# Kernel tuning notes

Measured on AMD Instinct MI355X. Metric: run time of the kernel, lower is better.

The kernel has to match this reference:

```python
import jax, jax.numpy as jnp
import numpy as np

B, T_PREFIX, C_IN = 8, 6144, 8
OUT_LEN, OUT_C = 2048, 8
AUX_DIM = 16
D_MODEL, D_STATE, HEADDIM, EXPAND = 256, 32, 64, 2
D_INNER = EXPAND * D_MODEL            # 512
NHEADS = D_INNER // HEADDIM           # 8
CONV_DIM = D_INNER + 2 * D_STATE      # 576
D_PROJ = 2 * D_INNER + 2 * D_STATE + NHEADS  # 1096
N_LAYERS = 2
CHUNK = 64
PATCH = 16
PRECONV_K = 5
DCONV_K = 4


def setup_inputs() -> dict:
    key = jax.random.key(0)
    ks = iter(jax.random.split(key, 64))
    def rn(shape, s=0.02):
        return s * jax.random.normal(next(ks), shape, jnp.float32)
    inp = dict(
        x_prefix=jax.random.normal(next(ks), (B, T_PREFIX, C_IN), jnp.float32),
        y_aux=jax.random.normal(next(ks), (B, AUX_DIM), jnp.float32),
        pre_conv_w=rn((D_MODEL, C_IN, PRECONV_K), 0.1),
        pre_conv_b=rn((D_MODEL,)),
        patch_w=rn((D_MODEL, D_MODEL, PATCH), 0.05),
        patch_b=rn((D_MODEL,)),
        mask_token=rn((D_MODEL,)),
        aux_w=rn((AUX_DIM, D_MODEL), 0.1),
        aux_b=rn((D_MODEL,)),
        patch_out_w=rn((2 * D_MODEL, OUT_C * PATCH), 0.05),
        patch_out_b=rn((OUT_C * PATCH,)),
    )
    for d in ('fwd', 'bwd'):
        inp[f'{d}_norm_w'] = jnp.ones((N_LAYERS, D_MODEL), jnp.float32)
        inp[f'{d}_inproj'] = rn((N_LAYERS, D_MODEL, D_PROJ), 0.05)
        inp[f'{d}_conv_w'] = rn((N_LAYERS, CONV_DIM, DCONV_K), 0.2)
        inp[f'{d}_conv_b'] = rn((N_LAYERS, CONV_DIM))
        inp[f'{d}_dtbias'] = rn((N_LAYERS, NHEADS), 0.5)
        inp[f'{d}_Alog'] = jnp.tile(jnp.log(jnp.arange(1, NHEADS + 1, dtype=jnp.float32)), (N_LAYERS, 1))
        inp[f'{d}_D'] = jnp.ones((N_LAYERS, NHEADS), jnp.float32)
        inp[f'{d}_gnorm'] = jnp.ones((N_LAYERS, D_INNER), jnp.float32)
        inp[f'{d}_outproj'] = rn((N_LAYERS, D_INNER, D_MODEL), 0.05)
    return inp


def rmsnorm(x, w, eps=1e-5):
    return x * jax.lax.rsqrt(jnp.mean(x * x, axis=-1, keepdims=True) + eps) * w


def conv1d(x, w, b, stride, pad):  # x: [B,C,T], w: [O,I,K]
    y = jax.lax.conv_general_dilated(x, w, (stride,), [(pad, pad)],
                                     dimension_numbers=('NCH', 'OIH', 'NCH'))
    return y + b[None, :, None]


def mamba_block(u, inproj, conv_w, conv_b, dtbias, Alog, Dp, gnorm_w, outproj):
    # Mamba-2/SSD style block: in_proj -> z | xBC | dt, causal depthwise conv,
    # selective scan with per-head scalar decay A, +D skip, gated RMSNorm, out_proj.
    b, T, _ = u.shape
    zxbcdt = u @ inproj                                   # [b,T,D_PROJ]
    z = zxbcdt[..., :D_INNER]
    xBC = zxbcdt[..., D_INNER:D_INNER + CONV_DIM]
    dt = jax.nn.softplus(zxbcdt[..., -NHEADS:] + dtbias)  # [b,T,H]
    # causal depthwise conv over time
    xc = jax.lax.conv_general_dilated(xBC.transpose(0, 2, 1), conv_w[:, None, :], (1,),
                                      [(DCONV_K - 1, 0)],
                                      dimension_numbers=('NCH', 'OIH', 'NCH'),
                                      feature_group_count=CONV_DIM)
    xBC = jax.nn.silu((xc + conv_b[None, :, None]).transpose(0, 2, 1))
    xs = xBC[..., :D_INNER].reshape(b, T, NHEADS, HEADDIM)  # [b,T,H,P]
    Bm = xBC[..., D_INNER:D_INNER + D_STATE]                # [b,T,N]
    Cm = xBC[..., D_INNER + D_STATE:]                       # [b,T,N]
    A = -jnp.exp(Alog)                                      # [H]

    def step(h, inps):  # h: [b,H,P,N]
        dt_t, x_t, B_t, C_t = inps
        dA = jnp.exp(dt_t * A)[:, :, None, None]
        h = h * dA + (dt_t[:, :, None] * x_t)[..., None] * B_t[:, None, None, :]
        y = jnp.einsum('bhpn,bn->bhp', h, C_t)
        return h, y

    h0 = jnp.zeros((b, NHEADS, HEADDIM, D_STATE), u.dtype)
    _, ys = jax.lax.scan(step, h0, (dt.transpose(1, 0, 2), xs.transpose(1, 0, 2, 3),
                                    Bm.transpose(1, 0, 2), Cm.transpose(1, 0, 2)))
    y = ys.transpose(1, 0, 2, 3) + Dp[None, None, :, None] * xs
    y = y.reshape(b, T, D_INNER)
    y = rmsnorm(y * jax.nn.silu(z), gnorm_w)
    return y @ outproj


def reference(x_prefix, y_aux, pre_conv_w, pre_conv_b, patch_w, patch_b, mask_token,
              aux_w, aux_b, fwd_norm_w, fwd_inproj, fwd_conv_w, fwd_conv_b, fwd_dtbias,
              fwd_Alog, fwd_D, fwd_gnorm, fwd_outproj, bwd_norm_w, bwd_inproj,
              bwd_conv_w, bwd_conv_b, bwd_dtbias, bwd_Alog, bwd_D, bwd_gnorm,
              bwd_outproj, patch_out_w, patch_out_b):
    b = x_prefix.shape[0]
    t_total = T_PREFIX + OUT_LEN
    x_full = jnp.pad(x_prefix, ((0, 0), (0, OUT_LEN), (0, 0)))        # zeros for future
    x = jax.nn.silu(conv1d(x_full.transpose(0, 2, 1), pre_conv_w, pre_conv_b, 1, PRECONV_K // 2))
    x = conv1d(x, patch_w, patch_b, PATCH, 0).transpose(0, 2, 1)      # [b, n_tokens, d_model]
    n_tokens = x.shape[1]
    # eval mode: deterministic future-patch mask, dropout is identity
    starts = jnp.arange(n_tokens) * PATCH
    mask = (starts >= T_PREFIX)[None, :, None]
    x = jnp.where(mask, mask_token[None, None, :], x)
    aux_bias = jax.nn.silu(y_aux @ aux_w + aux_b)[:, None, :]
    x = x + aux_bias
    pad_t = (-n_tokens) % CHUNK
    if pad_t:
        x = jnp.pad(x, ((0, 0), (0, pad_t), (0, 0)))
    h_f = x
    h_b = x[:, ::-1]
    for i in range(N_LAYERS):
        h_f = h_f + mamba_block(rmsnorm(h_f, fwd_norm_w[i]), fwd_inproj[i], fwd_conv_w[i],
                                fwd_conv_b[i], fwd_dtbias[i], fwd_Alog[i], fwd_D[i],
                                fwd_gnorm[i], fwd_outproj[i])
        h_b = h_b + mamba_block(rmsnorm(h_b, bwd_norm_w[i]), bwd_inproj[i], bwd_conv_w[i],
                                bwd_conv_b[i], bwd_dtbias[i], bwd_Alog[i], bwd_D[i],
                                bwd_gnorm[i], bwd_outproj[i])
    h = jnp.concatenate([h_f, h_b[:, ::-1]], axis=-1)[:, :n_tokens]   # [b,n,2*d_model]
    patch_pred = h @ patch_out_w + patch_out_b                        # [b,n,out_c*patch]
    y = patch_pred.reshape(b, n_tokens, OUT_C, PATCH).reshape(b, n_tokens * PATCH, OUT_C)
    y = y[:, :t_total, :]
    return y[:, T_PREFIX:, :]
```

## Files before the change

### kernel.cpp

```cpp
#include <hip/hip_runtime.h>
#include <hip/hip_bf16.h>
#include <math.h>

#define BSZ      8
#define TPREF    6144
#define CIN      8
#define DMODEL   256
#define DINNER   512
#define DSTATE   32
#define NHEADS   8
#define HEADDIM  64
#define CONVDIM  576
#define DPROJ    1096
#define ZXW      1088
#define NTOK     512
#define NVIS     384
#define TBWD     128
#define MFWD     (BSZ * NTOK)
#define MBWD     (BSZ * TBWD)
#define MALL     (MFWD + MBWD)

typedef float f32x4 __attribute__((ext_vector_type(4)));
typedef __bf16 bf16x8 __attribute__((ext_vector_type(8)));

__device__ __forceinline__ float silu_f(float x) { return x / (1.f + expf(-x)); }

#define ASYNC16(gp, lp) \
    __builtin_amdgcn_global_load_lds((const __attribute__((address_space(1))) void*)(gp), \
                                     (__attribute__((address_space(3))) void*)(lp), 16, 0, 0)

__global__ __launch_bounds__(256) void gemm_mfma(
    const __bf16* __restrict__ A, const __bf16* __restrict__ Bt,
    float* __restrict__ C, const float* __restrict__ bias,
    int N, int K, int ldc, int flags) {
    __shared__ char sm[16384];
    int tid = threadIdx.x;
    int m0 = blockIdx.y * 128, n0 = blockIdx.x * 128;
    int klen = K / gridDim.z;
    int kbeg = blockIdx.z * klen;
    int w = tid >> 6, l = tid & 63;
    int wm = w >> 1, wn = w & 1;
    int lm = l & 15, q = l >> 4;

    f32x4 acc[4][4];
    #pragma unroll
    for (int i = 0; i < 4; i++)
        #pragma unroll
        for (int j = 0; j < 4; j++) acc[i][j] = (f32x4)0.f;

    for (int k0 = 0; k0 < klen; k0 += 32) {
        int kb = kbeg + k0;
        #pragma unroll
        for (int i = 0; i < 2; i++) {
            int s = i * 256 + tid;
            ASYNC16(A + (size_t)(m0 + (s >> 2)) * K + kb + (s & 3) * 8, sm + s * 16);
        }
        #pragma unroll
        for (int i = 0; i < 2; i++) {
            int s = i * 256 + tid;
            ASYNC16(Bt + (size_t)(n0 + (s >> 2)) * K + kb + (s & 3) * 8, sm + 8192 + s * 16);
        }
        __syncthreads();
        bf16x8 af[4], bfr[4];
        #pragma unroll
        for (int mf = 0; mf < 4; mf++)
            af[mf] = *(const bf16x8*)(sm + (wm * 64 + mf * 16 + lm) * 64 + q * 16);
        #pragma unroll
        for (int nf = 0; nf < 4; nf++)
            bfr[nf] = *(const bf16x8*)(sm + 8192 + (wn * 64 + nf * 16 + lm) * 64 + q * 16);
        #pragma unroll
        for (int mf = 0; mf < 4; mf++)
            #pragma unroll
            for (int nf = 0; nf < 4; nf++)
                acc[mf][nf] = __builtin_amdgcn_mfma_f32_16x16x32_bf16(af[mf], bfr[nf], acc[mf][nf], 0, 0, 0);
        __syncthreads();
    }

    #pragma unroll
    for (int mf = 0; mf < 4; mf++) {
        int mbase = m0 + wm * 64 + mf * 16 + q * 4;
        #pragma unroll
        for (int nf = 0; nf < 4; nf++) {
            int n = n0 + wn * 64 + nf * 16 + lm;
            if (n < N) {
                #pragma unroll
                for (int r = 0; r < 4; r++) {
                    float v = acc[mf][nf][r];
                    if (flags & 4) {
                        v = silu_f(v + bias[n]);
                        ((__bf16*)C)[(size_t)(mbase + r) * ldc + n] = (__bf16)v;
                    } else if (flags & 16) {
                        int mm = mbase + r;
                        int bb = mm / NVIS, tk = mm - bb * NVIS;
                        atomicAdd(C + ((size_t)(bb * NTOK + tk)) * 256 + n, v);
                    } else if (flags & 2) {
                        atomicAdd(C + (size_t)(mbase + r) * ldc + n, v);
                    } else {
                        C[(size_t)(mbase + r) * ldc + n] = v;
                    }
                }
            }
        }
    }
}

__global__ __launch_bounds__(256) void preconv_gemm(
    const float* __restrict__ xp, const __bf16* __restrict__ WpreT,
    const float* __restrict__ bias, __bf16* __restrict__ Apatch) {
    __shared__ char sm[32768];
    int tid = threadIdx.x;
    int m0 = blockIdx.y * 128, n0 = blockIdx.x * 128;
    int w = tid >> 6, l = tid & 63;
    int wm = w >> 1, wn = w & 1, lm = l & 15, q = l >> 4;

    #pragma unroll
    for (int i = 0; i < 4; i++) {
        int s = i * 256 + tid;
        int kh = s >> 9, row = (s & 511) >> 2, within = s & 3;
        ASYNC16(WpreT + (size_t)(n0 + row) * 64 + kh * 32 + within * 8, sm + 16384 + s * 16);
    }
    if (tid < 128) {
        int m = m0 + tid;
        int b = m / TPREF, t = m - b * TPREF;
        __bf16 d[64];
        #pragma unroll
        for (int j = 40; j < 64; j++) d[j] = (__bf16)0.f;
        #pragma unroll
        for (int k = 0; k < 5; k++) {
            int tt = t - 2 + k;
            bool ok = (tt >= 0) && (tt < TPREF);
            const float* s = xp + ((size_t)b * TPREF + tt) * 8;
            #pragma unroll
            for (int i = 0; i < 8; i++)
                d[i * 5 + k] = ok ? (__bf16)s[i] : (__bf16)0.f;
        }
        uint4* o0 = (uint4*)(sm + tid * 64);
        uint4* o1 = (uint4*)(sm + 8192 + tid * 64);
        #pragma unroll
        for (int k = 0; k < 4; k++) { o0[k] = ((const uint4*)d)[k]; o1[k] = ((const uint4*)d)[4 + k]; }
    }
    __syncthreads();

    f32x4 acc[4][4];
    #pragma unroll
    for (int i = 0; i < 4; i++)
        #pragma unroll
        for (int j = 0; j < 4; j++) acc[i][j] = (f32x4)0.f;
    #pragma unroll
    for (int kh = 0; kh < 2; kh++) {
        bf16x8 af[4], bfr[4];
        #pragma unroll
        for (int mf = 0; mf < 4; mf++)
            af[mf] = *(const bf16x8*)(sm + kh * 8192 + (wm * 64 + mf * 16 + lm) * 64 + q * 16);
        #pragma unroll
        for (int nf = 0; nf < 4; nf++)
            bfr[nf] = *(const bf16x8*)(sm + 16384 + kh * 8192 + (wn * 64 + nf * 16 + lm) * 64 + q * 16);
        #pragma unroll
        for (int mf = 0; mf < 4; mf++)
            #pragma unroll
            for (int nf = 0; nf < 4; nf++)
                acc[mf][nf] = __builtin_amdgcn_mfma_f32_16x16x32_bf16(af[mf], bfr[nf], acc[mf][nf], 0, 0, 0);
    }
    #pragma unroll
    for (int mf = 0; mf < 4; mf++) {
        int mbase = m0 + wm * 64 + mf * 16 + q * 4;
        #pragma unroll
        for (int nf = 0; nf < 4; nf++) {
            int n = n0 + wn * 64 + nf * 16 + lm;
            #pragma unroll
            for (int r = 0; r < 4; r++) {
                float v = silu_f(acc[mf][nf][r] + bias[n]);
                Apatch[(size_t)(mbase + r) * 256 + n] = (__bf16)v;
            }
        }
    }
}

__global__ __launch_bounds__(256) void final_gemm(
    const float* __restrict__ h_all, const __bf16* __restrict__ poT,
    float* __restrict__ out) {
    __shared__ __bf16 Asm_[128][40];
    __shared__ char Bsm[8192];
    int tid = threadIdx.x;
    int m0 = blockIdx.y * 128;
    int z = blockIdx.z;
    int dir = z >> 1, kh = z & 1;
    int koff = kh * 128;
    int w = tid >> 6, l = tid & 63;
    int wm = w >> 1, wn_ = w & 1, lm = l & 15, q = l >> 4;
    f32x4 acc[4][4];
    #pragma unroll
    for (int i = 0; i < 4; i++)
        #pragma unroll
        for (int j = 0; j < 4; j++) acc[i][j] = (f32x4)0.f;

    int r = tid >> 1, half = tid & 1;
    int m = m0 + r;
    int b = m >> 7, jj = m & 127;
    size_t arow = (dir == 0) ? ((size_t)(b * NTOK + NVIS + jj) * 256)
                             : ((size_t)MFWD * 256 + (size_t)(b * TBWD + (TBWD - 1 - jj)) * 256);
    for (int k0 = 0; k0 < 128; k0 += 32) {
        {
            const float4* sp = (const float4*)(h_all + arow + koff + k0 + half * 16);
            float4 v0 = sp[0], v1 = sp[1], v2 = sp[2], v3 = sp[3];
            union { uint4 u; __bf16 hh[8]; } d0, d1;
            d0.hh[0] = (__bf16)v0.x; d0.hh[1] = (__bf16)v0.y; d0.hh[2] = (__bf16)v0.z; d0.hh[3] = (__bf16)v0.w;
            d0.hh[4] = (__bf16)v1.x; d0.hh[5] = (__bf16)v1.y; d0.hh[6] = (__bf16)v1.z; d0.hh[7] = (__bf16)v1.w;
            d1.hh[0] = (__bf16)v2.x; d1.hh[1] = (__bf16)v2.y; d1.hh[2] = (__bf16)v2.z; d1.hh[3] = (__bf16)v2.w;
            d1.hh[4] = (__bf16)v3.x; d1.hh[5] = (__bf16)v3.y; d1.hh[6] = (__bf16)v3.z; d1.hh[7] = (__bf16)v3.w;
            *(uint4*)&Asm_[r][half * 16] = d0.u;
            *(uint4*)&Asm_[r][half * 16 + 8] = d1.u;
        }
        #pragma unroll
        for (int i = 0; i < 2; i++) {
            int s = i * 256 + tid;
            ASYNC16(poT + (size_t)(s >> 2) * 512 + dir * 256 + koff + k0 + (s & 3) * 8, Bsm + s * 16);
        }
        __syncthreads();
        bf16x8 af[4], bfr[4];
        #pragma unroll
        for (int mf = 0; mf < 4; mf++)
            af[mf] = *(const bf16x8*)&Asm_[wm * 64 + mf * 16 + lm][q * 8];
        #pragma unroll
        for (int nf = 0; nf < 4; nf++)
            bfr[nf] = *(const bf16x8*)(Bsm + (wn_ * 64 + nf * 16 + lm) * 64 + q * 16);
        #pragma unroll
        for (int mf = 0; mf < 4; mf++)
            #pragma unroll
            for (int nf = 0; nf < 4; nf++)
                acc[mf][nf] = __builtin_amdgcn_mfma_f32_16x16x32_bf16(af[mf], bfr[nf], acc[mf][nf], 0, 0, 0);
        __syncthreads();
    }
    #pragma unroll
    for (int mf = 0; mf < 4; mf++) {
        int mbase = m0 + wm * 64 + mf * 16 + q * 4;
        #pragma unroll
        for (int nf = 0; nf < 4; nf++) {
            int n = wn_ * 64 + nf * 16 + lm;
            #pragma unroll
            for (int rr = 0; rr < 4; rr++)
                atomicAdd(out + (size_t)(mbase + rr) * 128 + n, acc[mf][nf][rr]);
        }
    }
}

__global__ __launch_bounds__(256) void gemm_inproj(
    const __bf16* __restrict__ u, const __bf16* __restrict__ ipTf,
    const __bf16* __restrict__ ipTb, __bf16* __restrict__ zxb, float* __restrict__ dtc) {
    __shared__ char sm[16384];
    int tid = threadIdx.x;
    int m0 = blockIdx.y * 128, n0 = blockIdx.x * 128;
    const __bf16* Bt = (m0 >= MFWD) ? ipTb : ipTf;
    int w = tid >> 6, l = tid & 63;
    int wm = w >> 1, wn = w & 1, lm = l & 15, q = l >> 4;
    f32x4 acc[4][4];
    #pragma unroll
    for (int i = 0; i < 4; i++)
        #pragma unroll
        for (int j = 0; j < 4; j++) acc[i][j] = (f32x4)0.f;
    for (int k0 = 0; k0 < 256; k0 += 32) {
        #pragma unroll
        for (int i = 0; i < 2; i++) {
            int s = i * 256 + tid;
            ASYNC16(u + (size_t)(m0 + (s >> 2)) * 256 + k0 + (s & 3) * 8, sm + s * 16);
        }
        #pragma unroll
        for (int i = 0; i < 2; i++) {
            int s = i * 256 + tid;
            ASYNC16(Bt + (size_t)(n0 + (s >> 2)) * 256 + k0 + (s & 3) * 8, sm + 8192 + s * 16);
        }
        __syncthreads();
        bf16x8 af[4], bfr[4];
        #pragma unroll
        for (int mf = 0; mf < 4; mf++)
            af[mf] = *(const bf16x8*)(sm + (wm * 64 + mf * 16 + lm) * 64 + q * 16);
        #pragma unroll
        for (int nf = 0; nf < 4; nf++)
            bfr[nf] = *(const bf16x8*)(sm + 8192 + (wn * 64 + nf * 16 + lm) * 64 + q * 16);
        #pragma unroll
        for (int mf = 0; mf < 4; mf++)
            #pragma unroll
            for (int nf = 0; nf < 4; nf++)
                acc[mf][nf] = __builtin_amdgcn_mfma_f32_16x16x32_bf16(af[mf], bfr[nf], acc[mf][nf], 0, 0, 0);
        __syncthreads();
    }
    #pragma unroll
    for (int mf = 0; mf < 4; mf++) {
        int mbase = m0 + wm * 64 + mf * 16 + q * 4;
        #pragma unroll
        for (int nf = 0; nf < 4; nf++) {
            int n = n0 + wn * 64 + nf * 16 + lm;
            #pragma unroll
            for (int r = 0; r < 4; r++) {
                float v = acc[mf][nf][r];
                if (n < ZXW) zxb[(size_t)(mbase + r) * ZXW + n] = (__bf16)v;
                else if (n < DPROJ) dtc[(size_t)(mbase + r) * 8 + (n - ZXW)] = v;
            }
        }
    }
}

__global__ __launch_bounds__(256) void gemm_outproj(
    const __bf16* __restrict__ y2, const __bf16* __restrict__ opTf,
    const __bf16* __restrict__ opTb, float* __restrict__ C, int layer) {
    __shared__ char sm[16384];
    int tid = threadIdx.x;
    int yb = blockIdx.y;
    int m0 = (layer == 0) ? yb * 128
                          : ((yb < 8) ? (yb * 512 + 384) : (MFWD + (yb - 8) * 128));
    int n0 = blockIdx.x * 128;
    const __bf16* Bt = (m0 >= MFWD) ? opTb : opTf;
    int w = tid >> 6, l = tid & 63;
    int wm = w >> 1, wn = w & 1, lm = l & 15, q = l >> 4;
    f32x4 acc[4][4];
    #pragma unroll
    for (int i = 0; i < 4; i++)
        #pragma unroll
        for (int j = 0; j < 4; j++) acc[i][j] = (f32x4)0.f;
    for (int k0 = 0; k0 < 512; k0 += 32) {
        #pragma unroll
        for (int i = 0; i < 2; i++) {
            int s = i * 256 + tid;
            ASYNC16(y2 + (size_t)(m0 + (s >> 2)) * 512 + k0 + (s & 3) * 8, sm + s * 16);
        }
        #pragma unroll
        for (int i = 0; i < 2; i++) {
            int s = i * 256 + tid;
            ASYNC16(Bt + (size_t)(n0 + (s >> 2)) * 512 + k0 + (s & 3) * 8, sm + 8192 + s * 16);
        }
        __syncthreads();
        bf16x8 af[4], bfr[4];
        #pragma unroll
        for (int mf = 0; mf < 4; mf++)
            af[mf] = *(const bf16x8*)(sm + (wm * 64 + mf * 16 + lm) * 64 + q * 16);
        #pragma unroll
        for (int nf = 0; nf < 4; nf++)
            bfr[nf] = *(const bf16x8*)(sm + 8192 + (wn * 64 + nf * 16 + lm) * 64 + q * 16);
        #pragma unroll
        for (int mf = 0; mf < 4; mf++)
            #pragma unroll
            for (int nf = 0; nf < 4; nf++)
                acc[mf][nf] = __builtin_amdgcn_mfma_f32_16x16x32_bf16(af[mf], bfr[nf], acc[mf][nf], 0, 0, 0);
        __syncthreads();
    }
    #pragma unroll
    for (int mf = 0; mf < 4; mf++) {
        int mbase = m0 + wm * 64 + mf * 16 + q * 4;
        #pragma unroll
        for (int nf = 0; nf < 4; nf++) {
            int n = n0 + wn * 64 + nf * 16 + lm;
            #pragma unroll
            for (int r = 0; r < 4; r++) {
                size_t ci = (size_t)(mbase + r) * DMODEL + n;
                C[ci] += acc[mf][nf][r];
            }
        }
    }
}

__global__ __launch_bounds__(256) void rmsnorm_all(
    const float* __restrict__ h, const float* __restrict__ wf,
    const float* __restrict__ wb, __bf16* __restrict__ u) {
    int row = blockIdx.x * 4 + (threadIdx.x >> 6);
    int lane = threadIdx.x & 63;
    const float* w = (row >= MFWD) ? wb : wf;
    float4 v = ((const float4*)(h + (size_t)row * 256))[lane];
    float ss = v.x * v.x + v.y * v.y + v.z * v.z + v.w * v.w;
    #pragma unroll
    for (int off = 32; off >= 1; off >>= 1) ss += __shfl_xor(ss, off);
    float rs = rsqrtf(ss * (1.f / 256.f) + 1e-5f);
    float4 wv = ((const float4*)w)[lane];
    __bf16 o4[4] = {(__bf16)(v.x * rs * wv.x), (__bf16)(v.y * rs * wv.y),
                    (__bf16)(v.z * rs * wv.z), (__bf16)(v.w * rs * wv.w)};
    *(uint2*)(u + (size_t)row * 256 + lane * 4) = *(uint2*)o4;
}

__global__ __launch_bounds__(256) void gatednorm_all(
    const __bf16* __restrict__ ysD, const __bf16* __restrict__ zxb,
    const float* __restrict__ gwf, const float* __restrict__ gwb,
    __bf16* __restrict__ y2) {
    int row = blockIdx.x * 4 + (threadIdx.x >> 6);
    int lane = threadIdx.x & 63;
    const float* gw = (row >= MFWD) ? gwb : gwf;
    union { uint4 u; __bf16 hh[8]; } yv, zv;
    yv.u = *(const uint4*)(ysD + (size_t)row * 512 + lane * 8);
    zv.u = *(const uint4*)(zxb + (size_t)row * ZXW + lane * 8);
    float g[8];
    #pragma unroll
    for (int j = 0; j < 8; j++) g[j] = (float)yv.hh[j] * silu_f((float)zv.hh[j]);
    float ss = 0.f;
    #pragma unroll
    for (int j = 0; j < 8; j++) ss += g[j] * g[j];
    #pragma unroll
    for (int off = 32; off >= 1; off >>= 1) ss += __shfl_xor(ss, off);
    float rs = rsqrtf(ss * (1.f / 512.f) + 1e-5f);
    const float4* gr = (const float4*)(gw + lane * 8);
    float4 g0 = gr[0], g1 = gr[1];
    union { uint4 u; __bf16 hh[8]; } d;
    d.hh[0] = (__bf16)(g[0] * rs * g0.x); d.hh[1] = (__bf16)(g[1] * rs * g0.y);
    d.hh[2] = (__bf16)(g[2] * rs * g0.z); d.hh[3] = (__bf16)(g[3] * rs * g0.w);
    d.hh[4] = (__bf16)(g[4] * rs * g1.x); d.hh[5] = (__bf16)(g[5] * rs * g1.y);
    d.hh[6] = (__bf16)(g[6] * rs * g1.z); d.hh[7] = (__bf16)(g[7] * rs * g1.w);
    *(uint4*)(y2 + (size_t)row * 512 + lane * 8) = d.u;
}

__global__ void prep_all(const float* __restrict__ pre_conv_w, const float* __restrict__ patch_w,
                         const float* __restrict__ ip0, const float* __restrict__ ip1,
                         const float* __restrict__ op0, const float* __restrict__ op1,
                         const float* __restrict__ pow_, const float* __restrict__ pob,
                         const float* __restrict__ y_aux, const float* __restrict__ aux_w,
                         const float* __restrict__ aux_b,
                         const float* __restrict__ patch_b, const float* __restrict__ mtok,
                         __bf16* __restrict__ WpreT, __bf16* __restrict__ WtT,
                         __bf16* __restrict__ inprojT, __bf16* __restrict__ outprojT,
                         __bf16* __restrict__ poT, float* __restrict__ dout,
                         float* __restrict__ h_all) {
    __shared__ float tile[32][33];
    int bx = blockIdx.x, tid = threadIdx.x;
    int tx = tid & 31, ty = tid >> 5;
    if (bx < 256) {
        int o = bx, c = tid;
        float f[16];
        const float4* s = (const float4*)(patch_w + (size_t)o * 4096 + c * 16);
        #pragma unroll
        for (int j = 0; j < 4; j++) *(float4*)&f[j * 4] = s[j];
        #pragma unroll
        for (int k = 0; k < 16; k++)
            WtT[(size_t)o * 4096 + k * 256 + c] = (__bf16)f[k];
        return;
    }
    bx -= 256;
    if (bx < 1152) {
        int seg = bx / 288, rem = bx % 288;
        int n0 = (rem / 8) * 32, k0 = (rem % 8) * 32;
        const float* src = (seg < 2 ? ip0 : ip1) + (size_t)(seg & 1) * 256 * DPROJ;
        #pragma unroll
        for (int j = 0; j < 4; j++) {
            int r = ty + j * 8;
            int n = n0 + tx;
            tile[r][tx] = (n < DPROJ) ? src[(size_t)(k0 + r) * DPROJ + n] : 0.f;
        }
        __syncthreads();
        __bf16* dst = inprojT + (size_t)seg * 1152 * 256;
        #pragma unroll
        for (int j = 0; j < 4; j++) {
            int r = ty + j * 8;
            dst[(size_t)(n0 + r) * 256 + k0 + tx] = (__bf16)tile[tx][r];
        }
        return;
    }
    bx -= 1152;
    if (bx < 512) {
        int s = bx / 128, rem = bx % 128;
        int n0 = (rem / 16) * 32, k0 = (rem % 16) * 32;
        const float* src = (s < 2 ? op0 : op1) + (size_t)(s & 1) * DINNER * DMODEL;
        #pragma unroll
        for (int j = 0; j < 4; j++) {
            int r = ty + j * 8;
            tile[r][tx] = src[(size_t)(k0 + r) * 256 + n0 + tx];
        }
        __syncthreads();
        __bf16* dst = outprojT + (size_t)s * 256 * 512;
        #pragma unroll
        for (int j = 0; j < 4; j++) {
            int r = ty + j * 8;
            dst[(size_t)(n0 + r) * 512 + k0 + tx] = (__bf16)tile[tx][r];
        }
        return;
    }
    bx -= 512;
    if (bx < 64) {
        int n0 = (bx / 16) * 32, k0 = (bx % 16) * 32;
        #pragma unroll
        for (int j = 0; j < 4; j++) {
            int r = ty + j * 8;
            tile[r][tx] = pow_[(size_t)(k0 + r) * 128 + n0 + tx];
        }
        __syncthreads();
        #pragma unroll
        for (int j = 0; j < 4; j++) {
            int r = ty + j * 8;
            poT[(size_t)(n0 + r) * 512 + k0 + tx] = (__bf16)tile[tx][r];
        }
        return;
    }
    bx -= 64;
    if (bx < 64) {
        int idx = bx * 256 + tid;
        int o = idx >> 6, kk = idx & 63;
        WpreT[idx] = (kk < 40) ? (__bf16)pre_conv_w[o * 40 + kk] : (__bf16)0.f;
        return;
    }
    bx -= 64;
    if (bx < 512) {
        int idx = bx * 256 + tid;
        dout[idx] = pob[idx & 127];
        return;
    }
    bx -= 512;
    {
        int row = bx, o = tid;
        int b; bool masked;
        if (row < MFWD) { b = row >> 9; int tok = row & 511; masked = (tok >= NVIS); }
        else { b = (row - MFWD) >> 7; masked = true; }
        float acc = aux_b[o];
        #pragma unroll
        for (int i = 0; i < 16; i++) acc += y_aux[b * 16 + i] * aux_w[i * 256 + o];
        float v = (masked ? mtok[o] : patch_b[o]) + silu_f(acc);
        h_all[(size_t)row * 256 + o] = v;
    }
}

__global__ __launch_bounds__(256) void dwconv2_kernel(
    const __bf16* __restrict__ zxb, const float* __restrict__ cwf, const float* __restrict__ cbf,
    const float* __restrict__ cwb, const float* __restrict__ cbb,
    __bf16* __restrict__ XtF, __bf16* __restrict__ XtB,
    __bf16* __restrict__ BCF, __bf16* __restrict__ BCB) {
    int cg = blockIdx.x;
    int id = blockIdx.y;
    int b, t0, T; size_t rowbase;
    const float *cw, *cb; __bf16 *Xt, *BC;
    if (id < 64) { b = id >> 3; t0 = (id & 7) * 64; T = NTOK; rowbase = (size_t)b * NTOK;
                   cw = cwf; cb = cbf; Xt = XtF; BC = BCF; }
    else { int i2 = id - 64; b = i2 >> 1; t0 = (i2 & 1) * 64; T = TBWD;
           rowbase = (size_t)MFWD + (size_t)b * TBWD; cw = cwb; cb = cbb; Xt = XtB; BC = BCB; }
    int c0 = cg * 64;
    __shared__ float xs[67][65];
    int lane = threadIdx.x & 63, grp = threadIdx.x >> 6;
    for (int r = grp; r < 67; r += 4) {
        int t = t0 - 3 + r;
        xs[r][lane] = (t >= 0) ? (float)zxb[(rowbase + t) * ZXW + DINNER + c0 + lane] : 0.f;
    }
    __syncthreads();
    if (cg < 8) {
        int t = lane;
        #pragma unroll
        for (int ci = grp; ci < 64; ci += 4) {
            int c = c0 + ci;
            float acc = cb[c];
            #pragma unroll
            for (int k = 0; k < 4; k++) acc += cw[c * 4 + k] * xs[t + k][ci];
            Xt[((size_t)((b * 8 + cg) * 64 + ci)) * T + t0 + t] = (__bf16)silu_f(acc);
        }
    } else {
        int c = lane;
        #pragma unroll
        for (int ti = grp; ti < 64; ti += 4) {
            float acc = cb[c0 + c];
            #pragma unroll
            for (int k = 0; k < 4; k++) acc += cw[(c0 + c) * 4 + k] * xs[ti + k][c];
            BC[((size_t)(b * T + t0 + ti)) * 64 + c] = (__bf16)silu_f(acc);
        }
    }
}

__global__ __launch_bounds__(64) void scan_local(
    const __bf16* __restrict__ XtF, const __bf16* __restrict__ XtB,
    const __bf16* __restrict__ BCF, const __bf16* __restrict__ BCB,
    const float* __restrict__ dtc,
    const float* __restrict__ dtbf, const float* __restrict__ dtbb,
    const float* __restrict__ Alogf, const float* __restrict__ Alogb,
    const float* __restrict__ Dpf, const float* __restrict__ Dpb,
    __bf16* __restrict__ ysD,
    __bf16* __restrict__ ChatF, __bf16* __restrict__ ChatB,
    float* __restrict__ dSF, float* __restrict__ dSB,
    float* __restrict__ DcsF, float* __restrict__ DcsB, int layer) {
    int id = blockIdx.x, hd = blockIdx.y;
    int b, c, T, NC; size_t rowbase;
    const __bf16 *Xt, *BC; __bf16* Chat; float *dS, *Dcs;
    const float *dtb, *Alog, *Dp;
    if (id < 64) { b = id >> 3; c = id & 7; T = NTOK; NC = 8; rowbase = (size_t)b * NTOK;
                   Xt = XtF; BC = BCF; Chat = ChatF; dS = dSF; Dcs = DcsF;
                   dtb = dtbf; Alog = Alogf; Dp = Dpf; }
    else { int i2 = id - 64; b = i2 >> 1; c = i2 & 1; T = TBWD; NC = 2;
           rowbase = (size_t)MFWD + (size_t)b * TBWD;
           Xt = XtB; BC = BCB; Chat = ChatB; dS = dSB; Dcs = DcsB;
           dtb = dtbb; Alog = Alogb; Dp = Dpb; }
    bool skipY = (layer == 1) && (id < 64) && (c < 6);
    int bh = b * 8 + hd;
    int t0 = c * 64;
    int lane = threadIdx.x;
    int lm = lane & 15, q = lane >> 4;
    float A = -expf(Alog[hd]);
    float Dh = Dp[hd];

    __shared__ char smem[23552];
    __bf16 (*Xl)[72]  = (__bf16(*)[72])(smem);
    __bf16 (*BCl)[72] = (__bf16(*)[72])(smem + 9216);
    __bf16 (*Pl)[72]  = (__bf16(*)[72])(smem + 9216);
    __bf16 (*Wbl)[72] = (__bf16(*)[72])(smem + 18432);
    float* lcs = (float*)(smem + 23040);
    float* dts = (float*)(smem + 23296);

    const uint4* xg = (const uint4*)(Xt + (size_t)(bh * 64 + lane) * T + t0);
    const uint4* bg = (const uint4*)(BC + ((size_t)(b * T + t0 + lane)) * 64);
    uint4 xv[8], bv[8];
    #pragma unroll
    for (int k = 0; k < 8; k++) { xv[k] = xg[k]; bv[k] = bg[k]; }
    float xdt = dtc[(rowbase + t0 + lane) * 8 + hd] + dtb[hd];
    float dtv = (xdt > 20.f) ? xdt : log1pf(expf(xdt));
    #pragma unroll
    for (int k = 0; k < 8; k++) {
        *(uint4*)&Xl[lane][k * 8] = xv[k];
        if (!skipY) *(uint4*)&BCl[lane][k * 8] = bv[k];
    }
    float lc = A * dtv;
    #pragma unroll
    for (int off = 1; off < 64; off <<= 1) {
        float o = __shfl_up(lc, off);
        if (lane >= off) lc += o;
    }
    lcs[lane] = lc; dts[lane] = dtv;
    float lc63 = __shfl(lc, 63);
    float wj = expf(lc63 - lc) * dtv;
    float eli = expf(lc);
    float Dc = expf(lc63);
    if (lane == 0) Dcs[bh * NC + c] = Dc;
    if (!skipY) {
        __bf16* co = Chat + ((size_t)(bh * NC + c) * 64 + lane) * 32;
        #pragma unroll
        for (int k = 0; k < 4; k++) {
            union { uint4 u; __bf16 h[8]; } s; s.u = bv[4 + k];
            union { uint4 u; __bf16 h[8]; } d;
            #pragma unroll
            for (int j = 0; j < 8; j++) d.h[j] = (__bf16)(eli * (float)s.h[j]);
            *(uint4*)(co + k * 8) = d.u;
        }
    }
    #pragma unroll
    for (int k = 0; k < 4; k++) {
        union { uint4 u; __bf16 h[8]; } s; s.u = bv[k];
        #pragma unroll
        for (int j = 0; j < 8; j++) Wbl[k * 8 + j][lane] = (__bf16)(wj * (float)s.h[j]);
    }
    __syncthreads();

    bf16x8 xf0[4], xf1[4];
    if (!skipY) {
        bf16x8 cfr[4], bfr[4];
        #pragma unroll
        for (int t4 = 0; t4 < 4; t4++) {
            cfr[t4] = *(const bf16x8*)&BCl[t4 * 16 + lm][32 + q * 8];
            bfr[t4] = *(const bf16x8*)&BCl[t4 * 16 + lm][q * 8];
        }
        #pragma unroll
        for (int ti = 0; ti < 4; ti++) {
            float lci[4];
            #pragma unroll
            for (int r = 0; r < 4; r++) lci[r] = lcs[ti * 16 + q * 4 + r];
            #pragma unroll
            for (int tj = 0; tj < 4; tj++) {
                if (tj > ti) {
                    #pragma unroll
                    for (int r = 0; r < 4; r++) Pl[ti * 16 + q * 4 + r][tj * 16 + lm] = (__bf16)0.f;
                    continue;
                }
                f32x4 g = __builtin_amdgcn_mfma_f32_16x16x32_bf16(cfr[ti], bfr[tj], (f32x4)0.f, 0, 0, 0);
                int j = tj * 16 + lm;
                float lcj = lcs[j], dtj = dts[j];
                #pragma unroll
                for (int r = 0; r < 4; r++) {
                    int i = ti * 16 + q * 4 + r;
                    float v = (j <= i) ? g[r] * expf(lci[r] - lcj) * dtj : 0.f;
                    if (j == i) v += Dh;
                    Pl[i][j] = (__bf16)v;
                }
            }
        }
        __syncthreads();

        bf16x8 pf0[4], pf1[4];
        #pragma unroll
        for (int t4 = 0; t4 < 4; t4++) {
            pf0[t4] = *(const bf16x8*)&Pl[t4 * 16 + lm][q * 8];
            pf1[t4] = *(const bf16x8*)&Pl[t4 * 16 + lm][32 + q * 8];
            xf0[t4] = *(const bf16x8*)&Xl[t4 * 16 + lm][q * 8];
            xf1[t4] = *(const bf16x8*)&Xl[t4 * 16 + lm][32 + q * 8];
        }
        #pragma unroll
        for (int ti = 0; ti < 4; ti++) {
            #pragma unroll
            for (int tp = 0; tp < 4; tp++) {
                f32x4 y = __builtin_amdgcn_mfma_f32_16x16x32_bf16(pf0[ti], xf0[tp], (f32x4)0.f, 0, 0, 0);
                y = __builtin_amdgcn_mfma_f32_16x16x32_bf16(pf1[ti], xf1[tp], y, 0, 0, 0);
                #pragma unroll
                for (int r = 0; r < 4; r++) {
                    int i = ti * 16 + q * 4 + r;
                    ysD[(rowbase + t0 + i) * DINNER + hd * 64 + tp * 16 + lm] = (__bf16)y[r];
                }
            }
        }
    } else {
        #pragma unroll
        for (int t4 = 0; t4 < 4; t4++) {
            xf0[t4] = *(const bf16x8*)&Xl[t4 * 16 + lm][q * 8];
            xf1[t4] = *(const bf16x8*)&Xl[t4 * 16 + lm][32 + q * 8];
        }
    }
    bf16x8 wf0[2], wf1[2];
    #pragma unroll
    for (int tn = 0; tn < 2; tn++) {
        wf0[tn] = *(const bf16x8*)&Wbl[tn * 16 + lm][q * 8];
        wf1[tn] = *(const bf16x8*)&Wbl[tn * 16 + lm][32 + q * 8];
    }
    float* dso = dS + (size_t)(bh * NC + c) * 2048;
    #pragma unroll
    for (int tp = 0; tp < 4; tp++) {
        #pragma unroll
        for (int tn = 0; tn < 2; tn++) {
            f32x4 s = __builtin_amdgcn_mfma_f32_16x16x32_bf16(xf0[tp], wf0[tn], (f32x4)0.f, 0, 0, 0);
            s = __builtin_amdgcn_mfma_f32_16x16x32_bf16(xf1[tp], wf1[tn], s, 0, 0, 0);
            #pragma unroll
            for (int r = 0; r < 4; r++) {
                int pp = tp * 16 + q * 4 + r, nn = tn * 16 + lm;
                dso[pp * 32 + nn] = s[r];
            }
        }
    }
}

__global__ __launch_bounds__(256) void scan_tail(
    const float* __restrict__ dSF, const float* __restrict__ dSB,
    const float* __restrict__ DcsF, const float* __restrict__ DcsB,
    const __bf16* __restrict__ ChatF, const __bf16* __restrict__ ChatB,
    __bf16* __restrict__ ysD, int layer) {
    int blk = blockIdx.x;
    int dir = blk >= 64;
    int bh = blk & 63;
    int NC = dir ? 2 : 8;
    int T = dir ? TBWD : NTOK;
    int b = bh >> 3, hd = bh & 7;
    size_t rowbase = dir ? ((size_t)MFWD + (size_t)b * TBWD) : ((size_t)b * NTOK);
    const float* dS = dir ? dSB : dSF;
    const float* Dcs = dir ? DcsB : DcsF;
    const __bf16* Chat = dir ? ChatB : ChatF;
    int cmin = (layer == 1 && !dir) ? 6 : 1;
    int tid = threadIdx.x;
    __shared__ __bf16 Spl[8][64][40];
    {
        int p = tid >> 2, n0 = (tid & 3) * 8;
        float S[8];
        #pragma unroll
        for (int j = 0; j < 8; j++) S[j] = 0.f;
        for (int c = 0; c < NC; c++) {
            union { uint4 u; __bf16 hh[8]; } o;
            #pragma unroll
            for (int j = 0; j < 8; j++) o.hh[j] = (__bf16)S[j];
            *(uint4*)&Spl[c][p][n0] = o.u;
            float Dc = Dcs[bh * NC + c];
            const float4* dp = (const float4*)(dS + ((size_t)(bh * NC + c)) * 2048 + tid * 8);
            float4 d0 = dp[0], d1 = dp[1];
            S[0] = Dc * S[0] + d0.x; S[1] = Dc * S[1] + d0.y;
            S[2] = Dc * S[2] + d0.z; S[3] = Dc * S[3] + d0.w;
            S[4] = Dc * S[4] + d1.x; S[5] = Dc * S[5] + d1.y;
            S[6] = Dc * S[6] + d1.z; S[7] = Dc * S[7] + d1.w;
        }
    }
    __syncthreads();
    int w = tid >> 6, l = tid & 63, lm = l & 15, q = l >> 4;
    for (int c = cmin + w; c < NC; c += 4) {
        int t0 = c * 64;
        const __bf16* Cb = Chat + (size_t)(bh * NC + c) * 2048;
        bf16x8 cf[4], sf[4];
        #pragma unroll
        for (int t4 = 0; t4 < 4; t4++) {
            cf[t4] = *(const bf16x8*)(Cb + (t4 * 16 + lm) * 32 + q * 8);
            sf[t4] = *(const bf16x8*)&Spl[c][t4 * 16 + lm][q * 8];
        }
        #pragma unroll
        for (int ti = 0; ti < 4; ti++) {
            #pragma unroll
            for (int tp = 0; tp < 4; tp++) {
                f32x4 y = __builtin_amdgcn_mfma_f32_16x16x32_bf16(cf[ti], sf[tp], (f32x4)0.f, 0, 0, 0);
                #pragma unroll
                for (int r = 0; r < 4; r++) {
                    int i = ti * 16 + q * 4 + r;
                    size_t idx = (rowbase + t0 + i) * DINNER + hd * 64 + tp * 16 + lm;
                    ysD[idx] = (__bf16)((float)ysD[idx] + y[r]);
                }
            }
        }
    }
}

extern "C" void kernel_launch(void* const* d_in, const int* in_sizes, int n_in,
                              void* d_out, int out_size, void* d_ws, size_t ws_size,
                              hipStream_t stream) {
    const float* x_prefix    = (const float*)d_in[0];
    const float* y_aux       = (const float*)d_in[1];
    const float* pre_conv_w  = (const float*)d_in[2];
    const float* pre_conv_b  = (const float*)d_in[3];
    const float* patch_w     = (const float*)d_in[4];
    const float* patch_b     = (const float*)d_in[5];
    const float* mask_token  = (const float*)d_in[6];
    const float* aux_w       = (const float*)d_in[7];
    const float* aux_b       = (const float*)d_in[8];
    const float* patch_out_w = (const float*)d_in[9];
    const float* patch_out_b = (const float*)d_in[10];
    const float* w_norm[2]   = {(const float*)d_in[11], (const float*)d_in[20]};
    const float* w_inproj[2] = {(const float*)d_in[12], (const float*)d_in[21]};
    const float* w_convw[2]  = {(const float*)d_in[13], (const float*)d_in[22]};
    const float* w_convb[2]  = {(const float*)d_in[14], (const float*)d_in[23]};
    const float* w_dtb[2]    = {(const float*)d_in[15], (const float*)d_in[24]};
    const float* w_alog[2]   = {(const float*)d_in[16], (const float*)d_in[25]};
    const float* w_D[2]      = {(const float*)d_in[17], (const float*)d_in[26]};
    const float* w_gnorm[2]  = {(const float*)d_in[18], (const float*)d_in[27]};
    const float* w_outproj[2]= {(const float*)d_in[19], (const float*)d_in[28]};

    char* p = (char*)d_ws;
    auto alloc = [&](size_t bytes) { char* r = p; p += (bytes + 255) & ~255ULL; return r; };
    __bf16* A_patch  = (__bf16*)alloc((size_t)3072 * 4096 * 2);
    __bf16* WpreT    = (__bf16*)alloc((size_t)256 * 64 * 2);
    __bf16* WtT      = (__bf16*)alloc((size_t)256 * 4096 * 2);
    __bf16* inprojT  = (__bf16*)alloc((size_t)4 * 1152 * 256 * 2);
    __bf16* outprojT = (__bf16*)alloc((size_t)4 * 256 * 512 * 2);
    __bf16* poT      = (__bf16*)alloc((size_t)128 * 512 * 2);
    float*  h_all    = (float*)alloc((size_t)MALL * 256 * 4);
    __bf16* u        = (__bf16*)alloc((size_t)MALL * 256 * 2);
    __bf16* zxb      = (__bf16*)alloc((size_t)MALL * ZXW * 2);
    float*  dtc      = (float*)alloc((size_t)MALL * 8 * 4);
    __bf16* XtF      = (__bf16*)alloc((size_t)64 * 64 * NTOK * 2);
    __bf16* XtB      = (__bf16*)alloc((size_t)64 * 64 * TBWD * 2);
    __bf16* BCF      = (__bf16*)alloc((size_t)BSZ * NTOK * 64 * 2);
    __bf16* BCB      = (__bf16*)alloc((size_t)BSZ * TBWD * 64 * 2);
    __bf16* ysD      = (__bf16*)alloc((size_t)MALL * DINNER * 2);
    __bf16* y2       = (__bf16*)alloc((size_t)MALL * DINNER * 2);
    __bf16* ChatF    = (__bf16*)alloc((size_t)64 * 8 * 2048 * 2);
    __bf16* ChatB    = (__bf16*)alloc((size_t)64 * 2 * 2048 * 2);
    float*  dSF      = (float*)alloc((size_t)64 * 8 * 2048 * 4);
    float*  dSB      = (float*)alloc((size_t)64 * 2 * 2048 * 4);
    float*  DcsF     = (float*)alloc((size_t)64 * 8 * 4);
    float*  DcsB     = (float*)alloc((size_t)64 * 2 * 4);

    prep_all<<<256 + 1152 + 512 + 64 + 64 + 512 + MALL, 256, 0, stream>>>(
        pre_conv_w, patch_w, w_inproj[0], w_inproj[1], w_outproj[0], w_outproj[1],
        patch_out_w, patch_out_b, y_aux, aux_w, aux_b, patch_b, mask_token,
        WpreT, WtT, inprojT, outprojT, poT, (float*)d_out, h_all);
    preconv_gemm<<<dim3(2, (BSZ * TPREF) / 128), 256, 0, stream>>>(
        x_prefix, WpreT, pre_conv_b, A_patch);
    gemm_mfma<<<dim3(2, 24, 8), 256, 0, stream>>>(
        A_patch, WtT, h_all, nullptr, 256, 4096, 256, 16);

    for (int i = 0; i < 2; i++) {
        const __bf16* ipTf = inprojT + (size_t)(0 * 2 + i) * 1152 * 256;
        const __bf16* ipTb = inprojT + (size_t)(1 * 2 + i) * 1152 * 256;
        const __bf16* opTf = outprojT + (size_t)(0 * 2 + i) * 256 * 512;
        const __bf16* opTb = outprojT + (size_t)(1 * 2 + i) * 256 * 512;
        rmsnorm_all<<<MALL / 4, 256, 0, stream>>>(h_all, w_norm[0] + i * 256, w_norm[1] + i * 256, u);
        gemm_inproj<<<dim3(9, MALL / 128), 256, 0, stream>>>(u, ipTf, ipTb, zxb, dtc);
        dwconv2_kernel<<<dim3(9, 80), 256, 0, stream>>>(
            zxb, w_convw[0] + i * CONVDIM * 4, w_convb[0] + i * CONVDIM,
            w_convw[1] + i * CONVDIM * 4, w_convb[1] + i * CONVDIM,
            XtF, XtB, BCF, BCB);
        scan_local<<<dim3(80, NHEADS), 64, 0, stream>>>(
            XtF, XtB, BCF, BCB, dtc,
            w_dtb[0] + i * 8, w_dtb[1] + i * 8,
            w_alog[0] + i * 8, w_alog[1] + i * 8,
            w_D[0] + i * 8, w_D[1] + i * 8,
            ysD, ChatF, ChatB, dSF, dSB, DcsF, DcsB, i);
        scan_tail<<<128, 256, 0, stream>>>(dSF, dSB, DcsF, DcsB, ChatF, ChatB, ysD, i);
        gatednorm_all<<<MALL / 4, 256, 0, stream>>>(
            ysD, zxb, w_gnorm[0] + i * DINNER, w_gnorm[1] + i * DINNER, y2);
        int oy = (i == 0) ? (MALL / 128) : 16;
        gemm_outproj<<<dim3(2, oy), 256, 0, stream>>>(y2, opTf, opTb, h_all, i);
    }

    final_gemm<<<dim3(1, 8, 4), 256, 0, stream>>>(h_all, poT, (float*)d_out);
}
```

Baseline: 325.0 us.

## Split scan_local chunk work across four wavefronts per block

The scan_local kernel moves from one 64-thread wavefront per chunk/head to four wavefronts. Each wave owns one 16-row tile for the P matrix, the Y product and the state-delta product. The shared-memory loads of X and B/C are spread over all 256 threads, and extra barriers are added between phases. The goal is to cut per-block serial latency in a small grid of 640 blocks. In exchange, every wave redundantly computes the cumulative-sum scan, and the added synchronization costs some time.

New measurement: 328.7 us. No clear change (+1.1%).

```diff
diff --git a/kernel.cpp b/kernel.cpp
--- a/kernel.cpp
+++ b/kernel.cpp
@@ -554,7 +554,7 @@
     }
 }
 
-__global__ __launch_bounds__(64) void scan_local(
+__global__ __launch_bounds__(256) void scan_local(
     const __bf16* __restrict__ XtF, const __bf16* __restrict__ XtB,
     const __bf16* __restrict__ BCF, const __bf16* __restrict__ BCB,
     const float* __restrict__ dtc,
@@ -579,8 +579,9 @@
     bool skipY = (layer == 1) && (id < 64) && (c < 6);
     int bh = b * 8 + hd;
     int t0 = c * 64;
-    int lane = threadIdx.x;
-    int lm = lane & 15, q = lane >> 4;
+    int tid = threadIdx.x;
+    int w = tid >> 6, l = tid & 63;
+    int lm = l & 15, q = l >> 4;
     float A = -expf(Alog[hd]);
     float Dh = Dp[hd];
 
@@ -592,109 +593,99 @@
     float* lcs = (float*)(smem + 23040);
     float* dts = (float*)(smem + 23296);
 
-    const uint4* xg = (const uint4*)(Xt + (size_t)(bh * 64 + lane) * T + t0);
-    const uint4* bg = (const uint4*)(BC + ((size_t)(b * T + t0 + lane)) * 64);
-    uint4 xv[8], bv[8];
-    #pragma unroll
-    for (int k = 0; k < 8; k++) { xv[k] = xg[k]; bv[k] = bg[k]; }
-    float xdt = dtc[(rowbase + t0 + lane) * 8 + hd] + dtb[hd];
+    {
+        int r = tid >> 2, seg = tid & 3;
+        const uint4* xg = (const uint4*)(Xt + (size_t)(bh * 64 + r) * T + t0) + seg * 2;
+        uint4 x0 = xg[0], x1 = xg[1];
+        const uint4* bg = (const uint4*)(BC + ((size_t)(b * T + t0 + r)) * 64) + seg * 2;
+        uint4 b0 = bg[0], b1 = bg[1];
+        *(uint4*)&Xl[r][seg * 16]      = x0;
+        *(uint4*)&Xl[r][seg * 16 + 8]  = x1;
+        *(uint4*)&BCl[r][seg * 16]     = b0;
+        *(uint4*)&BCl[r][seg * 16 + 8] = b1;
+    }
+    float xdt = dtc[(rowbase + t0 + l) * 8 + hd] + dtb[hd];
     float dtv = (xdt > 20.f) ? xdt : log1pf(expf(xdt));
-    #pragma unroll
-    for (int k = 0; k < 8; k++) {
-        *(uint4*)&Xl[lane][k * 8] = xv[k];
-        if (!skipY) *(uint4*)&BCl[lane][k * 8] = bv[k];
-    }
     float lc = A * dtv;
     #pragma unroll
     for (int off = 1; off < 64; off <<= 1) {
         float o = __shfl_up(lc, off);
-        if (lane >= off) lc += o;
-    }
-    lcs[lane] = lc; dts[lane] = dtv;
+        if (l >= off) lc += o;
+    }
     float lc63 = __shfl(lc, 63);
     float wj = expf(lc63 - lc) * dtv;
     float eli = expf(lc);
-    float Dc = expf(lc63);
-    if (lane == 0) Dcs[bh * NC + c] = Dc;
+    if (w == 0) {
+        lcs[l] = lc; dts[l] = dtv;
+        if (l == 0) Dcs[bh * NC + c] = expf(lc63);
+    }
+    __syncthreads();
+
     if (!skipY) {
-        __bf16* co = Chat + ((size_t)(bh * NC + c) * 64 + lane) * 32;
-        #pragma unroll
-        for (int k = 0; k < 4; k++) {
-            union { uint4 u; __bf16 h[8]; } s; s.u = bv[4 + k];
-            union { uint4 u; __bf16 h[8]; } d;
-            #pragma unroll
-            for (int j = 0; j < 8; j++) d.h[j] = (__bf16)(eli * (float)s.h[j]);
-            *(uint4*)(co + k * 8) = d.u;
-        }
-    }
-    #pragma unroll
-    for (int k = 0; k < 4; k++) {
-        union { uint4 u; __bf16 h[8]; } s; s.u = bv[k];
-        #pragma unroll
-        for (int j = 0; j < 8; j++) Wbl[k * 8 + j][lane] = (__bf16)(wj * (float)s.h[j]);
+        union { uint4 u; __bf16 h[8]; } s, d;
+        s.u = *(const uint4*)&BCl[l][32 + w * 8];
+        #pragma unroll
+        for (int j = 0; j < 8; j++) d.h[j] = (__bf16)(eli * (float)s.h[j]);
+        *(uint4*)(Chat + ((size_t)(bh * NC + c) * 64 + l) * 32 + w * 8) = d.u;
+    }
+    {
+        union { uint4 u; __bf16 h[8]; } s;
+        s.u = *(const uint4*)&BCl[l][w * 8];
+        #pragma unroll
+        for (int j = 0; j < 8; j++) Wbl[w * 8 + j][l] = (__bf16)(wj * (float)s.h[j]);
+    }
+    bf16x8 cfr, bfr[4];
+    if (!skipY) {
+        cfr = *(const bf16x8*)&BCl[w * 16 + lm][32 + q * 8];
+        #pragma unroll
+        for (int tj = 0; tj < 4; tj++)
+            if (tj <= w) bfr[tj] = *(const bf16x8*)&BCl[tj * 16 + lm][q * 8];
     }
     __syncthreads();
 
+    if (!skipY) {
+        float lci[4];
+        #pragma unroll
+        for (int r = 0; r < 4; r++) lci[r] = lcs[w * 16 + q * 4 + r];
+        #pragma unroll
+        for (int tj = 0; tj < 4; tj++) {
+            if (tj > w) {
+                #pragma unroll
+                for (int r = 0; r < 4; r++) Pl[w * 16 + q * 4 + r][tj * 16 + lm] = (__bf16)0.f;
+                continue;
+            }
+            f32x4 g = __builtin_amdgcn_mfma_f32_16x16x32_bf16(cfr, bfr[tj], (f32x4)0.f, 0, 0, 0);
+            int j = tj * 16 + lm;
+            float lcj = lcs[j], dtj = dts[j];
+            #pragma unroll
+            for (int r = 0; r < 4; r++) {
+                int i = w * 16 + q * 4 + r;
+                float v = (j <= i) ? g[r] * expf(lci[r] - lcj) * dtj : 0.f;
+                if (j == i) v += Dh;
+                Pl[i][j] = (__bf16)v;
+            }
+        }
+    }
+    __syncthreads();
+
     bf16x8 xf0[4], xf1[4];
+    #pragma unroll
+    for (int t4 = 0; t4 < 4; t4++) {
+        xf0[t4] = *(const bf16x8*)&Xl[t4 * 16 + lm][q * 8];
+        xf1[t4] = *(const bf16x8*)&Xl[t4 * 16 + lm][32 + q * 8];
+    }
     if (!skipY) {
-        bf16x8 cfr[4], bfr[4];
-        #pragma unroll
-        for (int t4 = 0; t4 < 4; t4++) {
-            cfr[t4] = *(const bf16x8*)&BCl[t4 * 16 + lm][32 + q * 8];
-            bfr[t4] = *(const bf16x8*)&BCl[t4 * 16 + lm][q * 8];
-        }
-        #pragma unroll
-        for (int ti = 0; ti < 4; ti++) {
-            float lci[4];
-            #pragma unroll
-            for (int r = 0; r < 4; r++) lci[r] = lcs[ti * 16 + q * 4 + r];
-            #pragma unroll
-            for (int tj = 0; tj < 4; tj++) {
-                if (tj > ti) {
-                    #pragma unroll
-                    for (int r = 0; r < 4; r++) Pl[ti * 16 + q * 4 + r][tj * 16 + lm] = (__bf16)0.f;
-                    continue;
-                }
-                f32x4 g = __builtin_amdgcn_mfma_f32_16x16x32_bf16(cfr[ti], bfr[tj], (f32x4)0.f, 0, 0, 0);
-                int j = tj * 16 + lm;
-                float lcj = lcs[j], dtj = dts[j];
-                #pragma unroll
-                for (int r = 0; r < 4; r++) {
-                    int i = ti * 16 + q * 4 + r;
-                    float v = (j <= i) ? g[r] * expf(lci[r] - lcj) * dtj : 0.f;
-                    if (j == i) v += Dh;
-                    Pl[i][j] = (__bf16)v;
-                }
+        bf16x8 pf0 = *(const bf16x8*)&Pl[w * 16 + lm][q * 8];
+        bf16x8 pf1 = *(const bf16x8*)&Pl[w * 16 + lm][32 + q * 8];
+        #pragma unroll
+        for (int tp = 0; tp < 4; tp++) {
+            f32x4 y = __builtin_amdgcn_mfma_f32_16x16x32_bf16(pf0, xf0[tp], (f32x4)0.f, 0, 0, 0);
+            y = __builtin_amdgcn_mfma_f32_16x16x32_bf16(pf1, xf1[tp], y, 0, 0, 0);
+            #pragma unroll
+            for (int r = 0; r < 4; r++) {
+                int i = w * 16 + q * 4 + r;
+                ysD[(rowbase + t0 + i) * DINNER + hd * 64 + tp * 16 + lm] = (__bf16)y[r];
             }
-        }
-        __syncthreads();
-
-        bf16x8 pf0[4], pf1[4];
-        #pragma unroll
-        for (int t4 = 0; t4 < 4; t4++) {
-            pf0[t4] = *(const bf16x8*)&Pl[t4 * 16 + lm][q * 8];
-            pf1[t4] = *(const bf16x8*)&Pl[t4 * 16 + lm][32 + q * 8];
-            xf0[t4] = *(const bf16x8*)&Xl[t4 * 16 + lm][q * 8];
-            xf1[t4] = *(const bf16x8*)&Xl[t4 * 16 + lm][32 + q * 8];
-        }
-        #pragma unroll
-        for (int ti = 0; ti < 4; ti++) {
-            #pragma unroll
-            for (int tp = 0; tp < 4; tp++) {
-                f32x4 y = __builtin_amdgcn_mfma_f32_16x16x32_bf16(pf0[ti], xf0[tp], (f32x4)0.f, 0, 0, 0);
-                y = __builtin_amdgcn_mfma_f32_16x16x32_bf16(pf1[ti], xf1[tp], y, 0, 0, 0);
-                #pragma unroll
-                for (int r = 0; r < 4; r++) {
-                    int i = ti * 16 + q * 4 + r;
-                    ysD[(rowbase + t0 + i) * DINNER + hd * 64 + tp * 16 + lm] = (__bf16)y[r];
-                }
-            }
-        }
-    } else {
-        #pragma unroll
-        for (int t4 = 0; t4 < 4; t4++) {
-            xf0[t4] = *(const bf16x8*)&Xl[t4 * 16 + lm][q * 8];
-            xf1[t4] = *(const bf16x8*)&Xl[t4 * 16 + lm][32 + q * 8];
         }
     }
     bf16x8 wf0[2], wf1[2];
@@ -705,16 +696,13 @@
     }
     float* dso = dS + (size_t)(bh * NC + c) * 2048;
     #pragma unroll
-    for (int tp = 0; tp < 4; tp++) {
-        #pragma unroll
-        for (int tn = 0; tn < 2; tn++) {
-            f32x4 s = __builtin_amdgcn_mfma_f32_16x16x32_bf16(xf0[tp], wf0[tn], (f32x4)0.f, 0, 0, 0);
-            s = __builtin_amdgcn_mfma_f32_16x16x32_bf16(xf1[tp], wf1[tn], s, 0, 0, 0);
-            #pragma unroll
-            for (int r = 0; r < 4; r++) {
-                int pp = tp * 16 + q * 4 + r, nn = tn * 16 + lm;
-                dso[pp * 32 + nn] = s[r];
-            }
+    for (int tn = 0; tn < 2; tn++) {
+        f32x4 s = __builtin_amdgcn_mfma_f32_16x16x32_bf16(xf0[w], wf0[tn], (f32x4)0.f, 0, 0, 0);
+        s = __builtin_amdgcn_mfma_f32_16x16x32_bf16(xf1[w], wf1[tn], s, 0, 0, 0);
+        #pragma unroll
+        for (int r = 0; r < 4; r++) {
+            int pp = w * 16 + q * 4 + r, nn = tn * 16 + lm;
+            dso[pp * 32 + nn] = s[r];
         }
     }
 }
@@ -852,7 +840,7 @@
             zxb, w_convw[0] + i * CONVDIM * 4, w_convb[0] + i * CONVDIM,
             w_convw[1] + i * CONVDIM * 4, w_convb[1] + i * CONVDIM,
             XtF, XtB, BCF, BCB);
-        scan_local<<<dim3(80, NHEADS), 64, 0, stream>>>(
+        scan_local<<<dim3(80, NHEADS), 256, 0, stream>>>(
             XtF, XtB, BCF, BCB, dtc,
             w_dtb[0] + i * 8, w_dtb[1] + i * 8,
             w_alog[0] + i * 8, w_alog[1] + i * 8,
```
